# Optimization experiments

Measured on AMD Instinct MI355X. Metric: run time of the kernel, lower is better.

The kernel has to match this reference:

```python
import jax, jax.numpy as jnp
import numpy as np


def setup_inputs() -> dict:
    key = jax.random.key(0)
    ks = jax.random.split(key, 7)
    B, T, C = 8, 2048, 1024
    s = 0.02
    return {
        "x": jax.random.normal(ks[0], (B, T, C), dtype=jnp.float32),
        "Wq": jax.random.normal(ks[1], (C, C), dtype=jnp.float32) * s,
        "bq": jax.random.normal(ks[2], (C,), dtype=jnp.float32) * s,
        "Wk": jax.random.normal(ks[3], (C, C), dtype=jnp.float32) * s,
        "bk": jax.random.normal(ks[4], (C,), dtype=jnp.float32) * s,
        "Wv": jax.random.normal(ks[5], (C, C), dtype=jnp.float32) * s,
        "bv": jax.random.normal(ks[6], (C,), dtype=jnp.float32) * s,
    }


def reference(x, Wq, bq, Wk, bk, Wv, bv):
    # Single-head causal self-attention: Linear QKV -> QK^T/sqrt(C) -> causal mask -> softmax -> @V
    B, T, C = x.shape
    q = x @ Wq.T + bq  # [B,T,C]  (torch Linear: x @ W^T + b)
    k = x @ Wk.T + bk
    v = x @ Wv.T + bv
    scale = jnp.asarray(C, x.dtype) ** -0.5
    att = jnp.einsum("btc,bsc->bts", q, k) * scale  # [B,T,T]
    causal = jnp.tril(jnp.ones((T, T), dtype=bool))
    att = jnp.where(causal, att, jnp.finfo(att.dtype).min)
    att = jax.nn.softmax(att, axis=-1)
    out = jnp.einsum("bts,bsc->btc", att, v)  # [B,T,C]
    return out
```

## Files before the change

### kernel.cpp

```cpp
#include <hip/hip_runtime.h>
#include <hip/hip_bf16.h>

typedef __attribute__((ext_vector_type(8))) short bf16x8;
typedef __attribute__((ext_vector_type(4))) float floatx4;
typedef __attribute__((ext_vector_type(4))) short short4v;

__device__ inline short f2bf(float f) {
  union { float f; unsigned u; } v; v.f = f;
  unsigned r = v.u + 0x7fffu + ((v.u >> 16) & 1u);
  return (short)(r >> 16);
}

__device__ inline void gload_lds16(const short* g, short* l) {
  __builtin_amdgcn_global_load_lds(
      (const __attribute__((address_space(1))) unsigned int*)g,
      (__attribute__((address_space(3))) unsigned int*)l, 16, 0, 0);
}

__global__ __launch_bounds__(256) void cvt_kernel(
    const float* __restrict__ x, const float* __restrict__ wq,
    const float* __restrict__ wk, const float* __restrict__ wv,
    short* __restrict__ Xb, short* __restrict__ Wb) {
  long i4 = (long)(blockIdx.x * 256 + threadIdx.x) * 4;
  const float* src; short* dst; long off;
  if (i4 < 16777216L) {
    src = x; dst = Xb; off = i4;
  } else {
    long j = i4 - 16777216L;
    int mat = (int)(j >> 20);
    src = (mat == 0) ? wq : ((mat == 1) ? wk : wv);
    dst = Wb + ((long)mat << 20);
    off = j & 1048575L;
  }
  float4 v = *(const float4*)(src + off);
  short4v o; o.x = f2bf(v.x); o.y = f2bf(v.y); o.z = f2bf(v.z); o.w = f2bf(v.w);
  *(short4v*)(dst + off) = o;
}

__global__ __launch_bounds__(512, 2) void qkv_gemm(
    const short* __restrict__ Xb, const short* __restrict__ Wb,
    const float* __restrict__ bq, const float* __restrict__ bk,
    const float* __restrict__ bv,
    short* __restrict__ Qf, short* __restrict__ Kf, short* __restrict__ Vf) {
  __shared__ short As[4 * 8192];
  __shared__ short Bs[4 * 8192];

  const int tid  = threadIdx.x;
  const int wave = tid >> 6, lane = tid & 63;
  const int quad = lane >> 4, l16 = lane & 15;
  const int wm = wave >> 2, wn = wave & 3;

  int bid = (int)blockIdx.x;
  bid = (bid & 7) * 96 + (bid >> 3);
  const int bx = bid / 12, by = bid % 12;
  const int row0 = bx * 256, colbase = by * 256;

  const int sr = tid >> 2;
  const int sx = (((tid & 3) ^ ((tid >> 3) & 3)) << 3);
  const short* gAbase = Xb + (size_t)(row0 + sr) * 1024 + sx;
  const short* gBbase = Wb + (size_t)(colbase + sr) * 1024 + sx;
  short* lA = (short*)As + tid * 8;
  short* lB = (short*)Bs + tid * 8;

#define STAGE_A(S) { const int _s = (S); const int _sl = (_s & 3) * 8192; \
  gload_lds16(gAbase + (size_t)_s * 32, lA + _sl); \
  gload_lds16(gAbase + (size_t)_s * 32 + 131072, lA + _sl + 4096); }
#define STAGE_B(S) { const int _s = (S); const int _sl = (_s & 3) * 8192; \
  gload_lds16(gBbase + (size_t)_s * 32, lB + _sl); \
  gload_lds16(gBbase + (size_t)_s * 32 + 131072, lB + _sl + 4096); }

  const int coff = (quad ^ ((l16 >> 1) & 3)) * 8;
  const int aRow = (wm * 128 + l16) * 32 + coff;
  const int bRow = (wn * 64 + l16) * 32 + coff;

  floatx4 acc[8][4] = {};

  STAGE_A(0) STAGE_B(0) STAGE_A(1) STAGE_B(1) STAGE_A(2) STAGE_B(2)
  asm volatile("s_waitcnt vmcnt(4)" ::: "memory");
  __builtin_amdgcn_s_barrier();

#define PHASE_BAR() do { __builtin_amdgcn_sched_barrier(0); \
                         __builtin_amdgcn_s_barrier(); } while (0)
#define MFMA_ROW(MT, AF) \
  acc[MT][0] = __builtin_amdgcn_mfma_f32_16x16x32_bf16(AF, bf0, acc[MT][0], 0, 0, 0); \
  acc[MT][1] = __builtin_amdgcn_mfma_f32_16x16x32_bf16(AF, bf1, acc[MT][1], 0, 0, 0); \
  acc[MT][2] = __builtin_amdgcn_mfma_f32_16x16x32_bf16(AF, bf2, acc[MT][2], 0, 0, 0); \
  acc[MT][3] = __builtin_amdgcn_mfma_f32_16x16x32_bf16(AF, bf3, acc[MT][3], 0, 0, 0);

#define STEP(S, WAIT) { \
  const int sl_ = ((S) & 3) * 8192; \
   \
  bf16x8 af0 = *(const bf16x8*)(As + sl_ + aRow); \
  bf16x8 af1 = *(const bf16x8*)(As + sl_ + aRow + 512); \
  bf16x8 af2 = *(const bf16x8*)(As + sl_ + aRow + 1024); \
  bf16x8 af3 = *(const bf16x8*)(As + sl_ + aRow + 1536); \
  bf16x8 bf0 = *(const bf16x8*)(Bs + sl_ + bRow); \
  bf16x8 bf1 = *(const bf16x8*)(Bs + sl_ + bRow + 512); \
  bf16x8 bf2 = *(const bf16x8*)(Bs + sl_ + bRow + 1024); \
  bf16x8 bf3 = *(const bf16x8*)(Bs + sl_ + bRow + 1536); \
  STAGE_A(((S) + 3) & 31) \
  PHASE_BAR(); \
  __builtin_amdgcn_s_setprio(1); \
  MFMA_ROW(0, af0) MFMA_ROW(1, af1) MFMA_ROW(2, af2) MFMA_ROW(3, af3) \
  __builtin_amdgcn_s_setprio(0); \
  PHASE_BAR(); \
   \
  bf16x8 ag0 = *(const bf16x8*)(As + sl_ + aRow + 2048); \
  bf16x8 ag1 = *(const bf16x8*)(As + sl_ + aRow + 2560); \
  bf16x8 ag2 = *(const bf16x8*)(As + sl_ + aRow + 3072); \
  bf16x8 ag3 = *(const bf16x8*)(As + sl_ + aRow + 3584); \
  STAGE_B(((S) + 3) & 31) \
  PHASE_BAR(); \
  __builtin_amdgcn_s_setprio(1); \
  MFMA_ROW(4, ag0) MFMA_ROW(5, ag1) MFMA_ROW(6, ag2) MFMA_ROW(7, ag3) \
  __builtin_amdgcn_s_setprio(0); \
  if (WAIT) { asm volatile("s_waitcnt vmcnt(4)" ::: "memory"); } \
  PHASE_BAR(); \
}

#pragma unroll 1
  for (int kt = 0; kt < 16; ++kt) {
    STEP(kt * 2, 0)
    STEP(kt * 2 + 1, 1)
  }

  const int mat = by >> 2;
  const float* bias = (mat == 0) ? bq : (mat == 1) ? bk : bv;
  const float qs = (mat == 0) ? 0.03125f : 1.0f;
  int cn[4]; float bb[4];
#pragma unroll
  for (int nb = 0; nb < 4; ++nb) {
    cn[nb] = ((by & 3) << 8) + wn * 64 + nb * 16 + l16;
    bb[nb] = bias[cn[nb]];
  }

  if (mat <= 1) {
    short* dst = (mat == 0) ? Qf : Kf;
#pragma unroll
    for (int mt = 0; mt < 8; ++mt) {
      const int rowb = row0 + wm * 128 + mt * 16 + quad * 4;
      const int bat = rowb >> 11, t0 = rowb & 2047;
#pragma unroll
      for (int nb = 0; nb < 4; ++nb) {
        const int c = cn[nb];
        const size_t base = ((((size_t)bat * 128 + (t0 >> 4)) * 32 + (c >> 5)) << 9)
                          + ((((c >> 3) & 3) * 16 + (t0 & 15)) << 3) + (c & 7);
#pragma unroll
        for (int r = 0; r < 4; ++r)
          dst[base + (size_t)r * 8] = f2bf((acc[mt][nb][r] + bb[nb]) * qs);
      }
    }
  } else {
#pragma unroll
    for (int mt = 0; mt < 8; ++mt) {
      const int rowb = row0 + wm * 128 + mt * 16 + quad * 4;
      const int bat = rowb >> 11, t0 = rowb & 2047;
#pragma unroll
      for (int nb = 0; nb < 4; ++nb) {
        const int c = cn[nb];
        const size_t base = ((((size_t)bat * 64 + (c >> 4)) * 64 + (t0 >> 5)) << 9)
                          + ((((t0 >> 3) & 3) * 16 + (c & 15)) << 3) + (t0 & 7);
        short4v ov;
#pragma unroll
        for (int r = 0; r < 4; ++r) ov[r] = f2bf(acc[mt][nb][r] + bb[nb]);
        *(short4v*)(Vf + base) = ov;
      }
    }
  }
#undef STEP
#undef MFMA_ROW
#undef PHASE_BAR
#undef STAGE_A
#undef STAGE_B
}

__global__ __launch_bounds__(512, 2) void flash_attn(
    const short* __restrict__ Qf, const short* __restrict__ Kf,
    const short* __restrict__ Vf, float* __restrict__ out) {
  __shared__ float Sf[8][32][68];
  __shared__ short Pb[32][72];
  __shared__ float arow[32];
  __shared__ float lrow[32];

  const int b   = blockIdx.x & 7;
  const int p   = blockIdx.x >> 3;
  const int tid = threadIdx.x;
  const int wave = tid >> 6, lane = tid & 63;
  const int quad = lane >> 4, l16 = lane & 15;
  const int row = tid >> 4, sub = tid & 15;

#pragma unroll 1
  for (int pass = 0; pass < 2; ++pass) {
    const int j = pass ? p : (63 - p);
    const int ntiles = (j >> 1) + 1;
    const int gr = j * 32 + row;

    bf16x8 qfr[2][4];
#pragma unroll
    for (int mt = 0; mt < 2; mt++) {
      const short* qp = Qf + ((((size_t)b * 128 + j * 2 + mt) * 32 + wave * 4) << 9) + lane * 8;
#pragma unroll
      for (int dc = 0; dc < 4; dc++)
        qfr[mt][dc] = *(const bf16x8*)(qp + ((size_t)dc << 9));
    }

    floatx4 O[2][8] = {};
    float m_i = -1e30f, l_i = 0.0f;

    for (int kt = 0; kt < ntiles; kt++) {
      const short* kp = Kf + ((((size_t)b * 128 + kt * 4) * 32 + wave * 4) << 9) + lane * 8;
      bf16x8 kb[4][4];
#pragma unroll
      for (int nt = 0; nt < 4; nt++)
#pragma unroll
        for (int dc = 0; dc < 4; dc++)
          kb[nt][dc] = *(const bf16x8*)(kp + (((size_t)nt * 32 + dc) << 9));

      floatx4 s[2][4] = {};
#pragma unroll
      for (int nt = 0; nt < 4; nt++)
#pragma unroll
        for (int dc = 0; dc < 4; dc++)
#pragma unroll
          for (int mt = 0; mt < 2; mt++)
            s[mt][nt] = __builtin_amdgcn_mfma_f32_16x16x32_bf16(qfr[mt][dc], kb[nt][dc], s[mt][nt], 0, 0, 0);

#pragma unroll
      for (int mt = 0; mt < 2; mt++)
#pragma unroll
        for (int nt = 0; nt < 4; nt++)
#pragma unroll
          for (int r = 0; r < 4; r++)
            Sf[wave][mt * 16 + quad * 4 + r][nt * 16 + l16] = s[mt][nt][r];
      __syncthreads();

      const short* vp = Vf + ((((size_t)b * 64 + wave * 8) * 64 + kt * 2) << 9) + lane * 8;
      bf16x8 vb[2][8];
#pragma unroll
      for (int nb = 0; nb < 8; nb++)
#pragma unroll
        for (int kc = 0; kc < 2; kc++)
          vb[kc][nb] = *(const bf16x8*)(vp + (((size_t)nb * 64 + kc) << 9));

      const int kvbase = kt * 64;
      floatx4 vsum = {};
#pragma unroll
      for (int w = 0; w < 8; w++)
        vsum += *(const floatx4*)&Sf[w][row][sub * 4];
      float sv[4], mx = -1e30f;
#pragma unroll
      for (int jj = 0; jj < 4; jj++) {
        float v = vsum[jj];
        if (kvbase + sub * 4 + jj > gr) v = -1e30f;
        sv[jj] = v;
        mx = fmaxf(mx, v);
      }
#pragma unroll
      for (int msk = 1; msk <= 8; msk <<= 1)
        mx = fmaxf(mx, __shfl_xor(mx, msk, 64));
      const float mn = fmaxf(m_i, mx);
      const float alpha = __expf(m_i - mn);
      m_i = mn;
      float ps = 0.0f;
      short4v pb4;
#pragma unroll
      for (int jj = 0; jj < 4; jj++) {
        float pe = __expf(sv[jj] - mn);
        ps += pe;
        pb4[jj] = f2bf(pe);
      }
      *(short4v*)&Pb[row][sub * 4] = pb4;
#pragma unroll
      for (int msk = 1; msk <= 8; msk <<= 1)
        ps += __shfl_xor(ps, msk, 64);
      l_i = l_i * alpha + ps;
      if (sub == 0) arow[row] = alpha;
      __syncthreads();

      float al[2][4];
#pragma unroll
      for (int mt = 0; mt < 2; mt++)
#pragma unroll
        for (int r = 0; r < 4; r++) al[mt][r] = arow[mt * 16 + quad * 4 + r];
#pragma unroll
      for (int mt = 0; mt < 2; mt++)
#pragma unroll
        for (int nb = 0; nb < 8; nb++)
#pragma unroll
          for (int r = 0; r < 4; r++) O[mt][nb][r] *= al[mt][r];

#pragma unroll
      for (int kc = 0; kc < 2; kc++)
#pragma unroll
        for (int mt = 0; mt < 2; mt++) {
          bf16x8 pa = *(const bf16x8*)&Pb[mt * 16 + l16][kc * 32 + quad * 8];
#pragma unroll
          for (int nb = 0; nb < 8; nb++)
            O[mt][nb] = __builtin_amdgcn_mfma_f32_16x16x32_bf16(pa, vb[kc][nb], O[mt][nb], 0, 0, 0);
        }
    }

    if (sub == 0) lrow[row] = 1.0f / l_i;
    __syncthreads();
    float linv[2][4];
#pragma unroll
    for (int mt = 0; mt < 2; mt++)
#pragma unroll
      for (int r = 0; r < 4; r++) linv[mt][r] = lrow[mt * 16 + quad * 4 + r];
#pragma unroll
    for (int mt = 0; mt < 2; mt++)
#pragma unroll
      for (int nb = 0; nb < 8; nb++)
#pragma unroll
        for (int r = 0; r < 4; r++) {
          const int rr = j * 32 + mt * 16 + quad * 4 + r;
          const int cc = wave * 128 + nb * 16 + l16;
          out[((size_t)b * 2048 + rr) * 1024 + cc] = O[mt][nb][r] * linv[mt][r];
        }
  }
}

extern "C" void kernel_launch(void* const* d_in, const int* in_sizes, int n_in,
                              void* d_out, int out_size, void* d_ws, size_t ws_size,
                              hipStream_t stream) {
  const float* x  = (const float*)d_in[0];
  const float* Wq = (const float*)d_in[1];
  const float* bq = (const float*)d_in[2];
  const float* Wk = (const float*)d_in[3];
  const float* bk = (const float*)d_in[4];
  const float* Wv = (const float*)d_in[5];
  const float* bv = (const float*)d_in[6];
  float* out = (float*)d_out;

  char* ws = (char*)d_ws;
  short* Xb = (short*)(ws);
  short* Wb = (short*)(ws + 33554432);
  short* Qf = (short*)(ws + 39845888);
  short* Kf = (short*)(ws + 73400320);
  short* Vf = (short*)(ws + 106954752);

  cvt_kernel<<<19456, 256, 0, stream>>>(x, Wq, Wk, Wv, Xb, Wb);
  qkv_gemm<<<dim3(768), 512, 0, stream>>>(Xb, Wb, bq, bk, bv, Qf, Kf, Vf);
  flash_attn<<<256, 512, 0, stream>>>(Qf, Kf, Vf, out);
}
```

Measured before the change: 386.1 us.

## Double-buffer K fragments in registers to prefetch next tile during attention

The flash-attention loop now keeps two register buffers for K fragments and loads the next tile's K while computing the current tile's QK^T, splitting the prefetch around the S-score stores. The loop is manually unrolled by two via a macro to swap buffers. The S computation is reorganised per mt to shorten accumulator lifetime, and a barrier is added at the end of each pass. This hides global-load latency at the cost of extra VGPRs under a 512-thread, 2-block launch bound, which may cause spills or lower occupancy.

```diff
diff --git a/kernel.cpp b/kernel.cpp
--- a/kernel.cpp
+++ b/kernel.cpp
@@ -89,7 +89,6 @@
 
 #define STEP(S, WAIT) { \
   const int sl_ = ((S) & 3) * 8192; \
-   \
   bf16x8 af0 = *(const bf16x8*)(As + sl_ + aRow); \
   bf16x8 af1 = *(const bf16x8*)(As + sl_ + aRow + 512); \
   bf16x8 af2 = *(const bf16x8*)(As + sl_ + aRow + 1024); \
@@ -104,7 +103,6 @@
   MFMA_ROW(0, af0) MFMA_ROW(1, af1) MFMA_ROW(2, af2) MFMA_ROW(3, af3) \
   __builtin_amdgcn_s_setprio(0); \
   PHASE_BAR(); \
-   \
   bf16x8 ag0 = *(const bf16x8*)(As + sl_ + aRow + 2048); \
   bf16x8 ag1 = *(const bf16x8*)(As + sl_ + aRow + 2560); \
   bf16x8 ag2 = *(const bf16x8*)(As + sl_ + aRow + 3072); \
@@ -189,6 +187,78 @@
   const int quad = lane >> 4, l16 = lane & 15;
   const int row = tid >> 4, sub = tid & 15;
 
+#define FA_ITER(CUR, NXT, KT) { \
+  const int kn_ = (KT) + 1; \
+  const bool pf_ = kn_ < ntiles; \
+  const short* kpn_ = Kf + ((((size_t)b * 128 + kn_ * 4) * 32 + wave * 4) << 9) + lane * 8; \
+  if (pf_) { \
+    _Pragma("unroll") for (int nt = 0; nt < 2; nt++) \
+      _Pragma("unroll") for (int dc = 0; dc < 4; dc++) \
+        NXT[nt][dc] = *(const bf16x8*)(kpn_ + (((size_t)(nt * 32 + dc)) << 9)); \
+  } \
+  _Pragma("unroll") for (int mt = 0; mt < 2; mt++) { \
+    floatx4 s4[4] = {}; \
+    _Pragma("unroll") for (int nt = 0; nt < 4; nt++) \
+      _Pragma("unroll") for (int dc = 0; dc < 4; dc++) \
+        s4[nt] = __builtin_amdgcn_mfma_f32_16x16x32_bf16(qfr[mt][dc], CUR[nt][dc], s4[nt], 0, 0, 0); \
+    _Pragma("unroll") for (int nt = 0; nt < 4; nt++) \
+      _Pragma("unroll") for (int r = 0; r < 4; r++) \
+        Sf[wave][mt * 16 + quad * 4 + r][nt * 16 + l16] = s4[nt][r]; \
+  } \
+  if (pf_) { \
+    _Pragma("unroll") for (int nt = 2; nt < 4; nt++) \
+      _Pragma("unroll") for (int dc = 0; dc < 4; dc++) \
+        NXT[nt][dc] = *(const bf16x8*)(kpn_ + (((size_t)(nt * 32 + dc)) << 9)); \
+  } \
+  __syncthreads();  \
+  const short* vp_ = Vf + ((((size_t)b * 64 + wave * 8) * 64 + (KT) * 2) << 9) + lane * 8; \
+  bf16x8 vb[2][8]; \
+  _Pragma("unroll") for (int nb = 0; nb < 8; nb++) \
+    _Pragma("unroll") for (int kc = 0; kc < 2; kc++) \
+      vb[kc][nb] = *(const bf16x8*)(vp_ + (((size_t)nb * 64 + kc) << 9)); \
+  const int kvbase_ = (KT) * 64; \
+  floatx4 vsum = {}; \
+  _Pragma("unroll") for (int w = 0; w < 8; w++) \
+    vsum += *(const floatx4*)&Sf[w][row][sub * 4]; \
+  float sv[4], mx = -1e30f; \
+  _Pragma("unroll") for (int jj = 0; jj < 4; jj++) { \
+    float v = vsum[jj]; \
+    if (kvbase_ + sub * 4 + jj > gr) v = -1e30f; \
+    sv[jj] = v; \
+    mx = fmaxf(mx, v); \
+  } \
+  _Pragma("unroll") for (int msk = 1; msk <= 8; msk <<= 1) \
+    mx = fmaxf(mx, __shfl_xor(mx, msk, 64)); \
+  const float mn = fmaxf(m_i, mx); \
+  const float alpha = __expf(m_i - mn); \
+  m_i = mn; \
+  float ps = 0.0f; \
+  short4v pb4; \
+  _Pragma("unroll") for (int jj = 0; jj < 4; jj++) { \
+    float pe = __expf(sv[jj] - mn); \
+    ps += pe; \
+    pb4[jj] = f2bf(pe); \
+  } \
+  *(short4v*)&Pb[row][sub * 4] = pb4; \
+  _Pragma("unroll") for (int msk = 1; msk <= 8; msk <<= 1) \
+    ps += __shfl_xor(ps, msk, 64); \
+  l_i = l_i * alpha + ps; \
+  if (sub == 0) arow[row] = alpha; \
+  __syncthreads();  \
+  float al[2][4]; \
+  _Pragma("unroll") for (int mt = 0; mt < 2; mt++) \
+    _Pragma("unroll") for (int r = 0; r < 4; r++) al[mt][r] = arow[mt * 16 + quad * 4 + r]; \
+  _Pragma("unroll") for (int mt = 0; mt < 2; mt++) \
+    _Pragma("unroll") for (int nb = 0; nb < 8; nb++) \
+      _Pragma("unroll") for (int r = 0; r < 4; r++) O[mt][nb][r] *= al[mt][r]; \
+  _Pragma("unroll") for (int kc = 0; kc < 2; kc++) \
+    _Pragma("unroll") for (int mt = 0; mt < 2; mt++) { \
+      bf16x8 pa = *(const bf16x8*)&Pb[mt * 16 + l16][kc * 32 + quad * 8]; \
+      _Pragma("unroll") for (int nb = 0; nb < 8; nb++) \
+        O[mt][nb] = __builtin_amdgcn_mfma_f32_16x16x32_bf16(pa, vb[kc][nb], O[mt][nb], 0, 0, 0); \
+    } \
+}
+
 #pragma unroll 1
   for (int pass = 0; pass < 2; ++pass) {
     const int j = pass ? p : (63 - p);
@@ -207,97 +277,22 @@
     floatx4 O[2][8] = {};
     float m_i = -1e30f, l_i = 0.0f;
 
-    for (int kt = 0; kt < ntiles; kt++) {
-      const short* kp = Kf + ((((size_t)b * 128 + kt * 4) * 32 + wave * 4) << 9) + lane * 8;
-      bf16x8 kb[4][4];
+    bf16x8 kbA[4][4], kbB[4][4];
+    {
+      const short* kp0 = Kf + (((size_t)b * 128 * 32 + wave * 4) << 9) + lane * 8;
 #pragma unroll
       for (int nt = 0; nt < 4; nt++)
 #pragma unroll
         for (int dc = 0; dc < 4; dc++)
-          kb[nt][dc] = *(const bf16x8*)(kp + (((size_t)nt * 32 + dc) << 9));
-
-      floatx4 s[2][4] = {};
-#pragma unroll
-      for (int nt = 0; nt < 4; nt++)
-#pragma unroll
-        for (int dc = 0; dc < 4; dc++)
-#pragma unroll
-          for (int mt = 0; mt < 2; mt++)
-            s[mt][nt] = __builtin_amdgcn_mfma_f32_16x16x32_bf16(qfr[mt][dc], kb[nt][dc], s[mt][nt], 0, 0, 0);
-
-#pragma unroll
-      for (int mt = 0; mt < 2; mt++)
-#pragma unroll
-        for (int nt = 0; nt < 4; nt++)
-#pragma unroll
-          for (int r = 0; r < 4; r++)
-            Sf[wave][mt * 16 + quad * 4 + r][nt * 16 + l16] = s[mt][nt][r];
-      __syncthreads();
-
-      const short* vp = Vf + ((((size_t)b * 64 + wave * 8) * 64 + kt * 2) << 9) + lane * 8;
-      bf16x8 vb[2][8];
-#pragma unroll
-      for (int nb = 0; nb < 8; nb++)
-#pragma unroll
-        for (int kc = 0; kc < 2; kc++)
-          vb[kc][nb] = *(const bf16x8*)(vp + (((size_t)nb * 64 + kc) << 9));
-
-      const int kvbase = kt * 64;
-      floatx4 vsum = {};
-#pragma unroll
-      for (int w = 0; w < 8; w++)
-        vsum += *(const floatx4*)&Sf[w][row][sub * 4];
-      float sv[4], mx = -1e30f;
-#pragma unroll
-      for (int jj = 0; jj < 4; jj++) {
-        float v = vsum[jj];
-        if (kvbase + sub * 4 + jj > gr) v = -1e30f;
-        sv[jj] = v;
-        mx = fmaxf(mx, v);
+          kbA[nt][dc] = *(const bf16x8*)(kp0 + (((size_t)(nt * 32 + dc)) << 9));
+    }
+
+#pragma unroll 1
+    for (int kt = 0; kt < ntiles; kt += 2) {
+      FA_ITER(kbA, kbB, kt)
+      if (kt + 1 < ntiles) {
+        FA_ITER(kbB, kbA, kt + 1)
       }
-#pragma unroll
-      for (int msk = 1; msk <= 8; msk <<= 1)
-        mx = fmaxf(mx, __shfl_xor(mx, msk, 64));
-      const float mn = fmaxf(m_i, mx);
-      const float alpha = __expf(m_i - mn);
-      m_i = mn;
-      float ps = 0.0f;
-      short4v pb4;
-#pragma unroll
-      for (int jj = 0; jj < 4; jj++) {
-        float pe = __expf(sv[jj] - mn);
-        ps += pe;
-        pb4[jj] = f2bf(pe);
-      }
-      *(short4v*)&Pb[row][sub * 4] = pb4;
-#pragma unroll
-      for (int msk = 1; msk <= 8; msk <<= 1)
-        ps += __shfl_xor(ps, msk, 64);
-      l_i = l_i * alpha + ps;
-      if (sub == 0) arow[row] = alpha;
-      __syncthreads();
-
-      float al[2][4];
-#pragma unroll
-      for (int mt = 0; mt < 2; mt++)
-#pragma unroll
-        for (int r = 0; r < 4; r++) al[mt][r] = arow[mt * 16 + quad * 4 + r];
-#pragma unroll
-      for (int mt = 0; mt < 2; mt++)
-#pragma unroll
-        for (int nb = 0; nb < 8; nb++)
-#pragma unroll
-          for (int r = 0; r < 4; r++) O[mt][nb][r] *= al[mt][r];
-
-#pragma unroll
-      for (int kc = 0; kc < 2; kc++)
-#pragma unroll
-        for (int mt = 0; mt < 2; mt++) {
-          bf16x8 pa = *(const bf16x8*)&Pb[mt * 16 + l16][kc * 32 + quad * 8];
-#pragma unroll
-          for (int nb = 0; nb < 8; nb++)
-            O[mt][nb] = __builtin_amdgcn_mfma_f32_16x16x32_bf16(pa, vb[kc][nb], O[mt][nb], 0, 0, 0);
-        }
     }
 
     if (sub == 0) lrow[row] = 1.0f / l_i;
@@ -317,7 +312,9 @@
           const int cc = wave * 128 + nb * 16 + l16;
           out[((size_t)b * 2048 + rr) * 1024 + cc] = O[mt][nb][r] * linv[mt][r];
         }
-  }
+    __syncthreads();
+  }
+#undef FA_ITER
 }
 
 extern "C" void kernel_launch(void* const* d_in, const int* in_sizes, int n_in,
```

New measurement: 693.6 us. 79.7% more time.
